# Kernel tuning notes

Hardware: AMD Instinct MI355X
Metric: run time of the kernel (lower is better)

## Reference

```python
import jax, jax.numpy as jnp
import numpy as np

CH, K, DIL = 256, 2, 8
B, T = 16, 4096
PAD = (K - 1) * DIL


def causal_conv(x, w, b, dilation):
    # x: [B, C, T], w: [O, I, K] (torch layout), b: [O]
    xp = jnp.pad(x, ((0, 0), (0, 0), (PAD, 0)))
    out = jax.lax.conv_general_dilated(
        xp, w, window_strides=(1,), padding='VALID',
        rhs_dilation=(dilation,),
        dimension_numbers=('NCH', 'OIH', 'NCH'))
    return out + b[None, :, None]


def conv1x1(x, w, b):
    # pointwise conv == channel matmul: [B,C,T] x [O,I]
    return jnp.einsum('oi,bit->bot', w[:, :, 0], x) + b[None, :, None]


def setup_inputs() -> dict:
    key = jax.random.key(0)
    ks = jax.random.split(key, 9)
    s_conv = 1.0 / np.sqrt(CH * K)
    s_1x1 = 1.0 / np.sqrt(CH)
    return {
        'x': jax.random.normal(ks[0], (B, CH, T), dtype=jnp.float32),
        'w_filter': jax.random.uniform(ks[1], (CH, CH, K), minval=-s_conv, maxval=s_conv),
        'b_filter': jax.random.uniform(ks[2], (CH,), minval=-s_conv, maxval=s_conv),
        'w_gate': jax.random.uniform(ks[3], (CH, CH, K), minval=-s_conv, maxval=s_conv),
        'b_gate': jax.random.uniform(ks[4], (CH,), minval=-s_conv, maxval=s_conv),
        'w_res': jax.random.uniform(ks[5], (CH, CH, 1), minval=-s_1x1, maxval=s_1x1),
        'b_res': jax.random.uniform(ks[6], (CH,), minval=-s_1x1, maxval=s_1x1),
        'w_skip': jax.random.uniform(ks[7], (CH, CH, 1), minval=-s_1x1, maxval=s_1x1),
        'b_skip': jax.random.uniform(ks[8], (CH,), minval=-s_1x1, maxval=s_1x1),
    }


def reference(x, w_filter, b_filter, w_gate, b_gate, w_res, b_res, w_skip, b_skip):
    f = jnp.tanh(causal_conv(x, w_filter, b_filter, DIL))
    g = jax.nn.sigmoid(causal_conv(x, w_gate, b_gate, DIL))
    z = f * g
    residual = conv1x1(z, w_res, b_res)
    skip = conv1x1(z, w_skip, b_skip)
    return (x + residual, skip)
```

## Files before the change

### kernel.cpp

```cpp
#include <hip/hip_runtime.h>

using f32x4 = __attribute__((ext_vector_type(4))) float;
using f32x2 = __attribute__((ext_vector_type(2))) float;
using s16x8 = __attribute__((ext_vector_type(8))) short;
using u16x4 = __attribute__((ext_vector_type(4))) ushort;

constexpr int NB   = 16;
constexpr int CH   = 256;
constexpr int TT   = 4096;
constexpr int NT   = 128;
constexpr int HALO = 8;
constexpr int XROWS = NT + HALO;
constexpr int ROWB = 528;
constexpr int XBYTES = XROWS * ROWB;
constexpr int ZOFF   = XBYTES;
constexpr int ZBYTES = NT * ROWB;

__device__ __forceinline__ ushort f2b(float f) {
    unsigned u; __builtin_memcpy(&u, &f, 4);
    u += 0x7FFFu + ((u >> 16) & 1u);
    return (ushort)(u >> 16);
}
__device__ __forceinline__ float fast_sigmoid(float x) {
    return __builtin_amdgcn_rcpf(1.f + __expf(-x));
}
__device__ __forceinline__ float fast_tanh(float x) {
    return 2.f * __builtin_amdgcn_rcpf(1.f + __expf(-2.f * x)) - 1.f;
}

__global__ __launch_bounds__(512)
void prep_w(const float* __restrict__ wf, const float* __restrict__ wg,
            const float* __restrict__ wr, const float* __restrict__ wsk,
            ushort* __restrict__ W1, ushort* __restrict__ W2) {
    int g = blockIdx.x * 512 + threadIdx.x;
    if (g < 512 * 64) {
        int m = g >> 6, i0 = (g & 63) * 4;
        const float* src = (m < 256) ? wf + ((size_t)m << 9)
                                     : wg + ((size_t)(m - 256) << 9);
        f32x4 a = *(const f32x4*)&src[i0 * 2];
        f32x4 c = *(const f32x4*)&src[i0 * 2 + 4];
        u16x4 t0v = { f2b(a[0]), f2b(a[2]), f2b(c[0]), f2b(c[2]) };
        u16x4 t1v = { f2b(a[1]), f2b(a[3]), f2b(c[1]), f2b(c[3]) };
        *(u16x4*)&W1[(size_t)m * 512 + i0]       = t0v;
        *(u16x4*)&W1[(size_t)m * 512 + 256 + i0] = t1v;
    } else {
        int g2 = g - 512 * 64;
        int m = g2 >> 6, i0 = (g2 & 63) * 4;
        const float* src = (m < 256) ? wr + ((size_t)m << 8)
                                     : wsk + ((size_t)(m - 256) << 8);
        f32x4 a = *(const f32x4*)&src[i0];
        u16x4 o = { f2b(a[0]), f2b(a[1]), f2b(a[2]), f2b(a[3]) };
        *(u16x4*)&W2[(size_t)m * 256 + i0] = o;
    }
}

__global__ __launch_bounds__(1024, 4)
void fused_block(const float* __restrict__ x,
                 const ushort* __restrict__ W1, const ushort* __restrict__ W2,
                 const float* __restrict__ b_filt, const float* __restrict__ b_gate,
                 const float* __restrict__ b_res,  const float* __restrict__ b_skip,
                 float* __restrict__ out) {
    __shared__ __align__(16) char lds[XBYTES + ZBYTES];

    const int tid = threadIdx.x;
    const int b  = blockIdx.x >> 5;
    const int t0 = (blockIdx.x & 31) * NT;
    const float* X = x + (size_t)b * CH * TT;
    const int tg0 = t0 - HALO;

    {
        const int tc  = tid & 7;
        const int cp  = tid >> 3;
        const float* Xa = X + (size_t)(cp * 2) * TT;
        const float* Xb = Xa + TT;
        #pragma unroll
        for (int it = 0; it < 4; ++it) {
            int tg = tg0 + it * 32 + tc * 4;
            f32x4 va = (f32x4){0.f,0.f,0.f,0.f}, vb = va;
            if (tg >= 0) { va = *(const f32x4*)&Xa[tg]; vb = *(const f32x4*)&Xb[tg]; }
            #pragma unroll
            for (int e = 0; e < 4; ++e) {
                int row = it * 32 + tc * 4 + e;
                unsigned pk = (unsigned)f2b(va[e]) | ((unsigned)f2b(vb[e]) << 16);
                *(unsigned*)(lds + row * ROWB + cp * 4) = pk;
            }
        }
        int c = tid & 255, h = tid >> 8;
        f32x2 v = *(const f32x2*)&X[(size_t)c * TT + tg0 + 128 + h * 2];
        #pragma unroll
        for (int e = 0; e < 2; ++e)
            *(ushort*)(lds + (128 + h * 2 + e) * ROWB + c * 2) = f2b(v[e]);
    }
    __syncthreads();

    const int wv = tid >> 6, lane = tid & 63;
    const int l16 = lane & 15, quad = lane >> 4;
    const int ch16 = wv * 16;
    const ushort* W1F = W1 + (size_t)(ch16 + l16) * 512 + quad * 8;
    const ushort* W1G = W1F + (size_t)256 * 512;
    const ushort* W2F = W2 + (size_t)(ch16 + l16) * 256 + quad * 8;
    const ushort* W2G = W2F + (size_t)256 * 256;

    const char* xbase = lds + l16 * ROWB + quad * 16;
    const char* zbase = lds + ZOFF + l16 * ROWB + quad * 16;

    f32x4 acc[8][2];
    #pragma unroll
    for (int i = 0; i < 8; ++i) { acc[i][0] = (f32x4){0.f,0.f,0.f,0.f};
                                  acc[i][1] = (f32x4){0.f,0.f,0.f,0.f}; }

    s16x8 wcF = *(const s16x8*)&W1F[0];
    s16x8 wcG = *(const s16x8*)&W1G[0];

    #pragma unroll
    for (int kq = 0; kq < 16; ++kq) {
        s16x8 wnF, wnG;
        if (kq < 15) {
            wnF = *(const s16x8*)&W1F[(kq + 1) * 32];
            wnG = *(const s16x8*)&W1G[(kq + 1) * 32];
        }
        const int tap = kq >> 3, ci = kq & 7;
        #pragma unroll
        for (int g = 0; g < 4; ++g) {
            s16x8 xf0 = *(const s16x8*)(xbase + (2*g)   * 8448 + tap * 4224 + ci * 64);
            s16x8 xf1 = *(const s16x8*)(xbase + (2*g+1) * 8448 + tap * 4224 + ci * 64);
            acc[2*g][0]   = __builtin_amdgcn_mfma_f32_16x16x32_bf16(xf0, wcF, acc[2*g][0],   0, 0, 0);
            acc[2*g][1]   = __builtin_amdgcn_mfma_f32_16x16x32_bf16(xf0, wcG, acc[2*g][1],   0, 0, 0);
            acc[2*g+1][0] = __builtin_amdgcn_mfma_f32_16x16x32_bf16(xf1, wcF, acc[2*g+1][0], 0, 0, 0);
            acc[2*g+1][1] = __builtin_amdgcn_mfma_f32_16x16x32_bf16(xf1, wcG, acc[2*g+1][1], 0, 0, 0);
        }
        if (kq < 15) { wcF = wnF; wcG = wnG; }
    }

    s16x8 wc2F = *(const s16x8*)&W2F[0];
    s16x8 wc2G = *(const s16x8*)&W2G[0];


    {
        const int zc = ch16 + l16;
        const float bfv = b_filt[zc], bgv = b_gate[zc];
        #pragma unroll
        for (int tm = 0; tm < 8; ++tm) {
            #pragma unroll
            for (int r = 0; r < 4; ++r) {
                float fv = acc[tm][0][r] + bfv;
                float gv = acc[tm][1][r] + bgv;
                int row = tm * 16 + quad * 4 + r;
                *(ushort*)(lds + ZOFF + row * ROWB + zc * 2) =
                    f2b(fast_tanh(fv) * fast_sigmoid(gv));
            }
        }
    }
    __syncthreads();

    #pragma unroll
    for (int i = 0; i < 8; ++i) { acc[i][0] = (f32x4){0.f,0.f,0.f,0.f};
                                  acc[i][1] = (f32x4){0.f,0.f,0.f,0.f}; }

    #pragma unroll
    for (int kq = 0; kq < 8; ++kq) {
        s16x8 wn2F, wn2G;
        if (kq < 7) {
            wn2F = *(const s16x8*)&W2F[(kq + 1) * 32];
            wn2G = *(const s16x8*)&W2G[(kq + 1) * 32];
        }
        #pragma unroll
        for (int g = 0; g < 4; ++g) {
            s16x8 zf0 = *(const s16x8*)(zbase + (2*g)   * 8448 + kq * 64);
            s16x8 zf1 = *(const s16x8*)(zbase + (2*g+1) * 8448 + kq * 64);
            acc[2*g][0]   = __builtin_amdgcn_mfma_f32_16x16x32_bf16(zf0, wc2F, acc[2*g][0],   0, 0, 0);
            acc[2*g][1]   = __builtin_amdgcn_mfma_f32_16x16x32_bf16(zf0, wc2G, acc[2*g][1],   0, 0, 0);
            acc[2*g+1][0] = __builtin_amdgcn_mfma_f32_16x16x32_bf16(zf1, wc2F, acc[2*g+1][0], 0, 0, 0);
            acc[2*g+1][1] = __builtin_amdgcn_mfma_f32_16x16x32_bf16(zf1, wc2G, acc[2*g+1][1], 0, 0, 0);
        }
        if (kq < 7) { wc2F = wn2F; wc2G = wn2G; }
    }

    const size_t OUT1 = (size_t)NB * CH * TT;
    {
        const int ch = ch16 + l16;
        const float br = b_res[ch], bs = b_skip[ch];
        const float* Xc = X + (size_t)ch * TT + t0;
        float* O0 = out + ((size_t)(b * CH + ch)) * TT + t0;
        float* O1 = O0 + OUT1;
        #pragma unroll
        for (int tm = 0; tm < 8; ++tm) {
            const int ttk = tm * 16 + quad * 4;
            f32x4 xv = *(const f32x4*)&Xc[ttk];
            f32x4 o0, o1;
            #pragma unroll
            for (int r = 0; r < 4; ++r) {
                o0[r] = xv[r] + acc[tm][0][r] + br;
                o1[r] = acc[tm][1][r] + bs;
            }
            *(f32x4*)&O0[ttk] = o0;
            *(f32x4*)&O1[ttk] = o1;
        }
    }
}

extern "C" void kernel_launch(void* const* d_in, const int* in_sizes, int n_in,
                              void* d_out, int out_size, void* d_ws, size_t ws_size,
                              hipStream_t stream) {
    const float* x   = (const float*)d_in[0];
    const float* wf  = (const float*)d_in[1];
    const float* bfi = (const float*)d_in[2];
    const float* wg  = (const float*)d_in[3];
    const float* bg  = (const float*)d_in[4];
    const float* wr  = (const float*)d_in[5];
    const float* br  = (const float*)d_in[6];
    const float* wsk = (const float*)d_in[7];
    const float* bs  = (const float*)d_in[8];

    ushort* W1 = (ushort*)d_ws;
    ushort* W2 = W1 + 512 * 512;

    prep_w<<<128, 512, 0, stream>>>(wf, wg, wr, wsk, W1, W2);

    const int nBlocks = NB * (TT / NT);
    fused_block<<<nBlocks, 1024, 0, stream>>>(x, W1, W2, bfi, bg, br, bs,
                                              (float*)d_out);
}
```

Measured before the change: 256.3 us.

## Switch GEMMs to 32x32x16 MFMA with 32-channel by 64-time warp tiles

Replaces the 16x16x32 bf16 MFMA tiling, where each wave owned 16 output channels across all 128 time steps, with 32x32x16 MFMA tiles. Each wave now owns 32 channels by 64 time steps. This halves the LDS activation reads per MFMA and uses the larger MFMA shape with its higher per-instruction throughput. The cost is that each wave now loads weights for 32 channels, and the output stores become more strided (4-float chunks at a stride of 8), which may hurt coalescing.

Measured after the change: 332.3 us. 29.6% more time.

```diff
diff --git a/kernel.cpp b/kernel.cpp
--- a/kernel.cpp
+++ b/kernel.cpp
@@ -1,9 +1,10 @@
 #include <hip/hip_runtime.h>
 
-using f32x4 = __attribute__((ext_vector_type(4))) float;
-using f32x2 = __attribute__((ext_vector_type(2))) float;
-using s16x8 = __attribute__((ext_vector_type(8))) short;
-using u16x4 = __attribute__((ext_vector_type(4))) ushort;
+using f32x4  = __attribute__((ext_vector_type(4)))  float;
+using f32x2  = __attribute__((ext_vector_type(2)))  float;
+using f32x16 = __attribute__((ext_vector_type(16))) float;
+using s16x8  = __attribute__((ext_vector_type(8)))  short;
+using u16x4  = __attribute__((ext_vector_type(4)))  ushort;
 
 constexpr int NB   = 16;
 constexpr int CH   = 256;
@@ -94,107 +95,116 @@
     __syncthreads();
 
     const int wv = tid >> 6, lane = tid & 63;
-    const int l16 = lane & 15, quad = lane >> 4;
-    const int ch16 = wv * 16;
-    const ushort* W1F = W1 + (size_t)(ch16 + l16) * 512 + quad * 8;
+    const int l32 = lane & 31, hi = lane >> 5;
+    const int stripe = wv & 7;
+    const int tb = (wv >> 3) * 64;
+    const int ch0 = stripe * 32;
+
+    const ushort* W1F = W1 + (size_t)(ch0 + l32) * 512 + hi * 8;
     const ushort* W1G = W1F + (size_t)256 * 512;
-    const ushort* W2F = W2 + (size_t)(ch16 + l16) * 256 + quad * 8;
-    const ushort* W2G = W2F + (size_t)256 * 256;
-
-    const char* xbase = lds + l16 * ROWB + quad * 16;
-    const char* zbase = lds + ZOFF + l16 * ROWB + quad * 16;
-
-    f32x4 acc[8][2];
-    #pragma unroll
-    for (int i = 0; i < 8; ++i) { acc[i][0] = (f32x4){0.f,0.f,0.f,0.f};
-                                  acc[i][1] = (f32x4){0.f,0.f,0.f,0.f}; }
+    const ushort* W2R = W2 + (size_t)(ch0 + l32) * 256 + hi * 8;
+    const ushort* W2S = W2R + (size_t)256 * 256;
+
+    const char* xbase = lds + (tb + l32) * ROWB + hi * 16;
+    const char* zbase = lds + ZOFF + (tb + l32) * ROWB + hi * 16;
+
+    f32x16 acc00, acc01, acc10, acc11;
+    #pragma unroll
+    for (int r = 0; r < 16; ++r) { acc00[r] = 0.f; acc01[r] = 0.f;
+                                   acc10[r] = 0.f; acc11[r] = 0.f; }
 
     s16x8 wcF = *(const s16x8*)&W1F[0];
     s16x8 wcG = *(const s16x8*)&W1G[0];
 
     #pragma unroll
-    for (int kq = 0; kq < 16; ++kq) {
+    for (int ks = 0; ks < 32; ++ks) {
         s16x8 wnF, wnG;
-        if (kq < 15) {
-            wnF = *(const s16x8*)&W1F[(kq + 1) * 32];
-            wnG = *(const s16x8*)&W1G[(kq + 1) * 32];
-        }
-        const int tap = kq >> 3, ci = kq & 7;
-        #pragma unroll
-        for (int g = 0; g < 4; ++g) {
-            s16x8 xf0 = *(const s16x8*)(xbase + (2*g)   * 8448 + tap * 4224 + ci * 64);
-            s16x8 xf1 = *(const s16x8*)(xbase + (2*g+1) * 8448 + tap * 4224 + ci * 64);
-            acc[2*g][0]   = __builtin_amdgcn_mfma_f32_16x16x32_bf16(xf0, wcF, acc[2*g][0],   0, 0, 0);
-            acc[2*g][1]   = __builtin_amdgcn_mfma_f32_16x16x32_bf16(xf0, wcG, acc[2*g][1],   0, 0, 0);
-            acc[2*g+1][0] = __builtin_amdgcn_mfma_f32_16x16x32_bf16(xf1, wcF, acc[2*g+1][0], 0, 0, 0);
-            acc[2*g+1][1] = __builtin_amdgcn_mfma_f32_16x16x32_bf16(xf1, wcG, acc[2*g+1][1], 0, 0, 0);
-        }
-        if (kq < 15) { wcF = wnF; wcG = wnG; }
-    }
-
-    s16x8 wc2F = *(const s16x8*)&W2F[0];
-    s16x8 wc2G = *(const s16x8*)&W2G[0];
+        if (ks < 31) {
+            wnF = *(const s16x8*)&W1F[(ks + 1) * 16];
+            wnG = *(const s16x8*)&W1G[(ks + 1) * 16];
+        }
+        const int tap = ks >> 4, ci = ks & 15;
+        s16x8 a0 = *(const s16x8*)(xbase + (tap * 8)      * ROWB + ci * 32);
+        s16x8 a1 = *(const s16x8*)(xbase + (32 + tap * 8) * ROWB + ci * 32);
+        acc00 = __builtin_amdgcn_mfma_f32_32x32x16_bf16(a0, wcF, acc00, 0, 0, 0);
+        acc01 = __builtin_amdgcn_mfma_f32_32x32x16_bf16(a0, wcG, acc01, 0, 0, 0);
+        acc10 = __builtin_amdgcn_mfma_f32_32x32x16_bf16(a1, wcF, acc10, 0, 0, 0);
+        acc11 = __builtin_amdgcn_mfma_f32_32x32x16_bf16(a1, wcG, acc11, 0, 0, 0);
+        if (ks < 31) { wcF = wnF; wcG = wnG; }
+    }
+
+    s16x8 wc2R = *(const s16x8*)&W2R[0];
+    s16x8 wc2S = *(const s16x8*)&W2S[0];
 
 
     {
-        const int zc = ch16 + l16;
+        const int zc = ch0 + l32;
         const float bfv = b_filt[zc], bgv = b_gate[zc];
-        #pragma unroll
-        for (int tm = 0; tm < 8; ++tm) {
-            #pragma unroll
-            for (int r = 0; r < 4; ++r) {
-                float fv = acc[tm][0][r] + bfv;
-                float gv = acc[tm][1][r] + bgv;
-                int row = tm * 16 + quad * 4 + r;
-                *(ushort*)(lds + ZOFF + row * ROWB + zc * 2) =
-                    f2b(fast_tanh(fv) * fast_sigmoid(gv));
-            }
+        char* zw = lds + ZOFF + zc * 2 + (tb + 4 * hi) * ROWB;
+        #pragma unroll
+        for (int r = 0; r < 16; ++r) {
+            float fv0 = acc00[r] + bfv, gv0 = acc01[r] + bgv;
+            int row0 = ((r & 3) + 8 * (r >> 2)) * ROWB;
+            *(ushort*)(zw + row0) = f2b(fast_tanh(fv0) * fast_sigmoid(gv0));
+            float fv1 = acc10[r] + bfv, gv1 = acc11[r] + bgv;
+            *(ushort*)(zw + row0 + 32 * ROWB) = f2b(fast_tanh(fv1) * fast_sigmoid(gv1));
         }
     }
     __syncthreads();
 
     #pragma unroll
-    for (int i = 0; i < 8; ++i) { acc[i][0] = (f32x4){0.f,0.f,0.f,0.f};
-                                  acc[i][1] = (f32x4){0.f,0.f,0.f,0.f}; }
-
-    #pragma unroll
-    for (int kq = 0; kq < 8; ++kq) {
-        s16x8 wn2F, wn2G;
-        if (kq < 7) {
-            wn2F = *(const s16x8*)&W2F[(kq + 1) * 32];
-            wn2G = *(const s16x8*)&W2G[(kq + 1) * 32];
-        }
-        #pragma unroll
-        for (int g = 0; g < 4; ++g) {
-            s16x8 zf0 = *(const s16x8*)(zbase + (2*g)   * 8448 + kq * 64);
-            s16x8 zf1 = *(const s16x8*)(zbase + (2*g+1) * 8448 + kq * 64);
-            acc[2*g][0]   = __builtin_amdgcn_mfma_f32_16x16x32_bf16(zf0, wc2F, acc[2*g][0],   0, 0, 0);
-            acc[2*g][1]   = __builtin_amdgcn_mfma_f32_16x16x32_bf16(zf0, wc2G, acc[2*g][1],   0, 0, 0);
-            acc[2*g+1][0] = __builtin_amdgcn_mfma_f32_16x16x32_bf16(zf1, wc2F, acc[2*g+1][0], 0, 0, 0);
-            acc[2*g+1][1] = __builtin_amdgcn_mfma_f32_16x16x32_bf16(zf1, wc2G, acc[2*g+1][1], 0, 0, 0);
-        }
-        if (kq < 7) { wc2F = wn2F; wc2G = wn2G; }
+    for (int r = 0; r < 16; ++r) { acc00[r] = 0.f; acc01[r] = 0.f;
+                                   acc10[r] = 0.f; acc11[r] = 0.f; }
+
+    #pragma unroll
+    for (int ks = 0; ks < 16; ++ks) {
+        s16x8 wnR, wnS;
+        if (ks < 15) {
+            wnR = *(const s16x8*)&W2R[(ks + 1) * 16];
+            wnS = *(const s16x8*)&W2S[(ks + 1) * 16];
+        }
+        s16x8 a0 = *(const s16x8*)(zbase + ks * 32);
+        s16x8 a1 = *(const s16x8*)(zbase + 32 * ROWB + ks * 32);
+        acc00 = __builtin_amdgcn_mfma_f32_32x32x16_bf16(a0, wc2R, acc00, 0, 0, 0);
+        acc01 = __builtin_amdgcn_mfma_f32_32x32x16_bf16(a0, wc2S, acc01, 0, 0, 0);
+        acc10 = __builtin_amdgcn_mfma_f32_32x32x16_bf16(a1, wc2R, acc10, 0, 0, 0);
+        acc11 = __builtin_amdgcn_mfma_f32_32x32x16_bf16(a1, wc2S, acc11, 0, 0, 0);
+        if (ks < 15) { wc2R = wnR; wc2S = wnS; }
     }
 
     const size_t OUT1 = (size_t)NB * CH * TT;
     {
-        const int ch = ch16 + l16;
+        const int ch = ch0 + l32;
         const float br = b_res[ch], bs = b_skip[ch];
-        const float* Xc = X + (size_t)ch * TT + t0;
-        float* O0 = out + ((size_t)(b * CH + ch)) * TT + t0;
+        const float* Xc = X + (size_t)ch * TT + t0 + tb + hi * 4;
+        float* O0 = out + ((size_t)(b * CH + ch)) * TT + t0 + tb + hi * 4;
         float* O1 = O0 + OUT1;
         #pragma unroll
-        for (int tm = 0; tm < 8; ++tm) {
-            const int ttk = tm * 16 + quad * 4;
-            f32x4 xv = *(const f32x4*)&Xc[ttk];
-            f32x4 o0, o1;
-            #pragma unroll
-            for (int r = 0; r < 4; ++r) {
-                o0[r] = xv[r] + acc[tm][0][r] + br;
-                o1[r] = acc[tm][1][r] + bs;
+        for (int q = 0; q < 4; ++q) {
+            {
+                const int toff = q * 8;
+                f32x4 xv = *(const f32x4*)&Xc[toff];
+                f32x4 o0, o1;
+                #pragma unroll
+                for (int j = 0; j < 4; ++j) {
+                    o0[j] = xv[j] + acc00[q * 4 + j] + br;
+                    o1[j] = acc01[q * 4 + j] + bs;
+                }
+                *(f32x4*)&O0[toff] = o0;
+                *(f32x4*)&O1[toff] = o1;
             }
-            *(f32x4*)&O0[ttk] = o0;
-            *(f32x4*)&O1[ttk] = o1;
+            {
+                const int toff = 32 + q * 8;
+                f32x4 xv = *(const f32x4*)&Xc[toff];
+                f32x4 o0, o1;
+                #pragma unroll
+                for (int j = 0; j < 4; ++j) {
+                    o0[j] = xv[j] + acc10[q * 4 + j] + br;
+                    o1[j] = acc11[q * 4 + j] + bs;
+                }
+                *(f32x4*)&O0[toff] = o0;
+                *(f32x4*)&O1[toff] = o1;
+            }
         }
     }
 }
```
